# Performance work log

Measured on AMD Instinct MI355X. Metric: run time of the kernel, lower is better.

The kernel has to match this reference:

```python
import jax, jax.numpy as jnp
import numpy as np
from jax import lax
from jax.scipy.special import logsumexp

NUM_TAGS = 5
B, L = 16384, 512


def setup_inputs() -> dict:
    key = jax.random.key(0)
    k1, k2, k3, k4, k5 = jax.random.split(key, 5)
    emissions = jax.random.normal(k1, (B, L, NUM_TAGS), dtype=jnp.float32)
    tags = jax.random.randint(k2, (B, L), 0, NUM_TAGS)
    mask = jnp.ones((B, L), dtype=bool)
    # learned CRF parameters, init U(-0.1, 0.1) as in reset_parameters
    transitions = jax.random.uniform(k3, (NUM_TAGS, NUM_TAGS), minval=-0.1, maxval=0.1, dtype=jnp.float32)
    start_transitions = jax.random.uniform(k4, (NUM_TAGS,), minval=-0.1, maxval=0.1, dtype=jnp.float32)
    end_transitions = jax.random.uniform(k5, (NUM_TAGS,), minval=-0.1, maxval=0.1, dtype=jnp.float32)
    return {
        "emissions": emissions,
        "transitions": transitions,
        "start_transitions": start_transitions,
        "end_transitions": end_transitions,
        "tags": tags,
        "mask": mask,
    }


def reference(emissions, transitions, start_transitions, end_transitions, tags, mask):
    """CRF mean negative log-likelihood: log_partition - gold_score (both batch means)."""
    Bs, Ls, C = emissions.shape
    maskf = mask.astype(emissions.dtype)

    # ---- log partition (forward algorithm); note: original torch code's
    # mask application here is a no-op (where(mask, s, s)), reproduced faithfully.
    init_score = start_transitions[None, :] + emissions[:, 0]  # (B, C)

    def step(score, em_i):
        # score: (B, C) over previous tag; em_i: (B, C)
        nxt = logsumexp(score[:, :, None] + transitions[None, :, :] + em_i[:, None, :], axis=1)
        return nxt, None

    ems = jnp.swapaxes(emissions[:, 1:], 0, 1)  # (L-1, B, C)
    final_score, _ = lax.scan(step, init_score, ems)
    log_den = logsumexp(final_score + end_transitions[None, :], axis=1).mean()

    # ---- gold path score (fully vectorized over time)
    s0 = start_transitions[tags[:, 0]] + jnp.take_along_axis(emissions[:, 0], tags[:, :1], axis=1)[:, 0]
    trans_scores = transitions[tags[:, :-1], tags[:, 1:]]  # (B, L-1)
    em_at_tags = jnp.take_along_axis(emissions, tags[:, :, None], axis=2)[:, :, 0]  # (B, L)
    path_score = s0 + ((trans_scores + em_at_tags[:, 1:]) * maskf[:, 1:]).sum(axis=1)
    last_idx = mask.sum(axis=1).astype(jnp.int32) - 1  # (B,)
    last_tags = jnp.take_along_axis(tags, last_idx[:, None], axis=1)[:, 0]
    log_num = (path_score + end_transitions[last_tags]).mean()

    return log_den - log_num
```

## Files before the change

### kernel.cpp

```cpp
#include <hip/hip_runtime.h>

#define NTAGS 5
#define BATCH 16384
#define SEQL 512
#define NCHUNK 8
#define CHUNKL 64
#define TT 8
#define NTILE (CHUNKL / TT)
#define RECF 32

__device__ __forceinline__ float f4c(float4 v, int c) {
    switch (c & 3) { case 0: return v.x; case 1: return v.y; case 2: return v.z; default: return v.w; }
}
__device__ __forceinline__ int i4c(int4 v, int c) {
    switch (c & 3) { case 0: return v.x; case 1: return v.y; case 2: return v.z; default: return v.w; }
}
__device__ __forceinline__ float sel5v(float a0, float a1, float a2, float a3, float a4, int t) {
    float r = a0;
    r = (t == 1) ? a1 : r;
    r = (t == 2) ? a2 : r;
    r = (t == 3) ? a3 : r;
    r = (t == 4) ? a4 : r;
    return r;
}

struct P1State {
    float M[25];
    float logS;
    float path;
    int prev;
};

__device__ __forceinline__ void p1_tile(const float4* tb, const int4* tg, bool sk0,
                                        P1State& st, const float eT[25],
                                        const float* ldsT, const float stR[5]) {
#pragma unroll
    for (int t = 0; t < TT; ++t) {
#define EMX(j) f4c(tb[(t * 5 + (j)) >> 2], (t * 5 + (j)) & 3)
        const float e0 = EMX(0), e1 = EMX(1), e2 = EMX(2), e3 = EMX(3), e4 = EMX(4);
#undef EMX
        const int tag = i4c(tg[t >> 2], t & 3);
        if (sk0 && t == 0) {
            st.path += sel5v(stR[0], stR[1], stR[2], stR[3], stR[4], tag) +
                       sel5v(e0, e1, e2, e3, e4, tag);
            st.prev = tag;
        } else {
            const float ex0 = __expf(e0), ex1 = __expf(e1), ex2 = __expf(e2),
                        ex3 = __expf(e3), ex4 = __expf(e4);
#pragma unroll
            for (int i = 0; i < 5; ++i) {
                const float m0 = st.M[i * 5 + 0], m1 = st.M[i * 5 + 1], m2 = st.M[i * 5 + 2],
                            m3 = st.M[i * 5 + 3], m4 = st.M[i * 5 + 4];
#pragma unroll
                for (int j = 0; j < 5; ++j) {
                    float a = m0 * eT[j];
                    a = fmaf(m1, eT[5 + j], a);
                    a = fmaf(m2, eT[10 + j], a);
                    a = fmaf(m3, eT[15 + j], a);
                    a = fmaf(m4, eT[20 + j], a);
                    const float exj = (j == 0) ? ex0 : (j == 1) ? ex1 : (j == 2) ? ex2
                                     : (j == 3) ? ex3 : ex4;
                    st.M[i * 5 + j] = a * exj;
                }
            }
            st.path += ldsT[st.prev * 5 + tag] + sel5v(e0, e1, e2, e3, e4, tag);
            st.prev = tag;
        }
        if ((t & 3) == 3) {
            float m = st.M[0];
#pragma unroll
            for (int i = 1; i < 25; ++i) m = fmaxf(m, st.M[i]);
            st.logS += __logf(m);
            const float rc = __builtin_amdgcn_rcpf(m);
#pragma unroll
            for (int i = 0; i < 25; ++i) st.M[i] *= rc;
        }
    }
}

__global__ __launch_bounds__(256, 2) void crf_phase1(
    const float* __restrict__ emis, const float* __restrict__ trans,
    const float* __restrict__ startT, const int* __restrict__ tags,
    float* __restrict__ ws) {
    __shared__ float ldsT[25];
    const int tid = threadIdx.x;
    if (tid < 25) ldsT[tid] = trans[tid];
    __syncthreads();

    float eT[25];
#pragma unroll
    for (int i = 0; i < 25; ++i) eT[i] = __expf(trans[i]);
    float stR[5];
#pragma unroll
    for (int j = 0; j < 5; ++j) stR[j] = startT[j];

    const int gt = blockIdx.x * 256 + tid;
    const int seq = gt >> 3;
    const int chunk = gt & 7;
    const bool first = (chunk == 0);

    const float4* esrc =
        (const float4*)(emis + (size_t)seq * (SEQL * NTAGS) + chunk * (CHUNKL * NTAGS));
    const int tbase = seq * SEQL + chunk * CHUNKL;
    const int4* tsrc = (const int4*)(tags + tbase);

    P1State st;
#pragma unroll
    for (int i = 0; i < 25; ++i) st.M[i] = 0.f;
    st.M[0] = st.M[6] = st.M[12] = st.M[18] = st.M[24] = 1.f;
    st.logS = 0.f;
    st.path = 0.f;
    st.prev = 0;
    if (!first) st.prev = tags[tbase - 1];

    float4 tA[10], tB[10];
    int4 gA[2], gB[2];
#pragma unroll
    for (int k = 0; k < 10; ++k) tA[k] = esrc[k];
    gA[0] = tsrc[0];
    gA[1] = tsrc[1];

#pragma unroll 1
    for (int tp = 0; tp < NTILE; tp += 2) {
        {
            const float4* ep = esrc + (tp + 1) * 10;
#pragma unroll
            for (int k = 0; k < 10; ++k) tB[k] = ep[k];
            const int4* tq = tsrc + (tp + 1) * 2;
            gB[0] = tq[0];
            gB[1] = tq[1];
        }
        p1_tile(tA, gA, first && (tp == 0), st, eT, ldsT, stR);
        {
            const int nx = (tp + 2 < NTILE) ? tp + 2 : tp;
            const float4* ep = esrc + nx * 10;
#pragma unroll
            for (int k = 0; k < 10; ++k) tA[k] = ep[k];
            const int4* tq = tsrc + nx * 2;
            gA[0] = tq[0];
            gA[1] = tq[1];
        }
        p1_tile(tB, gB, false, st, eT, ldsT, stR);
    }

    float4* rec = (float4*)(ws + (size_t)gt * RECF);
#pragma unroll
    for (int k = 0; k < 6; ++k)
        rec[k] = make_float4(st.M[4 * k], st.M[4 * k + 1], st.M[4 * k + 2], st.M[4 * k + 3]);
    rec[6] = make_float4(st.M[24], st.logS, st.path, 0.f);
}

__device__ __forceinline__ void p2_combine(const float4 r[7], float v[5], float& logZ,
                                           float& path) {
#define MM(i, j) f4c(r[((i) * 5 + (j)) >> 2], ((i) * 5 + (j)) & 3)
    float nv[5];
#pragma unroll
    for (int j = 0; j < 5; ++j) {
        float a = v[0] * MM(0, j);
        a = fmaf(v[1], MM(1, j), a);
        a = fmaf(v[2], MM(2, j), a);
        a = fmaf(v[3], MM(3, j), a);
        a = fmaf(v[4], MM(4, j), a);
        nv[j] = a;
    }
#undef MM
    logZ += r[6].y;
    path += r[6].z;
    const float m = fmaxf(fmaxf(fmaxf(nv[0], nv[1]), fmaxf(nv[2], nv[3])), nv[4]);
    logZ += __logf(m);
    const float rc = __builtin_amdgcn_rcpf(m);
#pragma unroll
    for (int j = 0; j < 5; ++j) v[j] = nv[j] * rc;
}

__global__ __launch_bounds__(256, 1) void crf_phase2(
    const float* __restrict__ emis, const float* __restrict__ startT,
    const float* __restrict__ endT, const int* __restrict__ tags,
    const float* __restrict__ ws, float* __restrict__ out) {
    const int seq = blockIdx.x * 256 + threadIdx.x;
    const float* eb = emis + (size_t)seq * (SEQL * NTAGS);
    const float4 e03 = *(const float4*)eb;
    const float e4v = eb[4];
    const float s0 = startT[0] + e03.x, s1 = startT[1] + e03.y, s2 = startT[2] + e03.z,
                s3 = startT[3] + e03.w, s4 = startT[4] + e4v;
    const float m0 = fmaxf(fmaxf(fmaxf(s0, s1), fmaxf(s2, s3)), s4);
    float v[5] = {__expf(s0 - m0), __expf(s1 - m0), __expf(s2 - m0), __expf(s3 - m0),
                  __expf(s4 - m0)};
    float logZ = m0, path = 0.f;

    const float4* wsb = (const float4*)(ws + (size_t)seq * NCHUNK * RECF);
    float4 rA[7], rB[7];
#pragma unroll
    for (int k = 0; k < 7; ++k) rA[k] = wsb[k];

#pragma unroll 1
    for (int c = 0; c < NCHUNK; c += 2) {
#pragma unroll
        for (int k = 0; k < 7; ++k) rB[k] = wsb[(c + 1) * 8 + k];
        p2_combine(rA, v, logZ, path);
        const int nx = (c + 2 < NCHUNK) ? c + 2 : c;
#pragma unroll
        for (int k = 0; k < 7; ++k) rA[k] = wsb[nx * 8 + k];
        p2_combine(rB, v, logZ, path);
    }

    const float en0 = endT[0], en1 = endT[1], en2 = endT[2], en3 = endT[3], en4 = endT[4];
    float sden = v[0] * __expf(en0);
    sden = fmaf(v[1], __expf(en1), sden);
    sden = fmaf(v[2], __expf(en2), sden);
    sden = fmaf(v[3], __expf(en3), sden);
    sden = fmaf(v[4], __expf(en4), sden);
    const float den = logZ + __logf(sden);

    const int lastTag = tags[seq * SEQL + (SEQL - 1)];
    const float num = path + sel5v(en0, en1, en2, en3, en4, lastTag);

    float val = (den - num) * (1.0f / (float)BATCH);
#pragma unroll
    for (int off = 32; off > 0; off >>= 1) val += __shfl_xor(val, off, 64);
    if ((threadIdx.x & 63) == 0) atomicAdd(out, val);
}

extern "C" void kernel_launch(void* const* d_in, const int* in_sizes, int n_in,
                              void* d_out, int out_size, void* d_ws, size_t ws_size,
                              hipStream_t stream) {
    const float* emis = (const float*)d_in[0];
    const float* trans = (const float*)d_in[1];
    const float* startT = (const float*)d_in[2];
    const float* endT = (const float*)d_in[3];
    const int* tags = (const int*)d_in[4];
    float* out = (float*)d_out;
    float* ws = (float*)d_ws;

    hipMemsetAsync(out, 0, sizeof(float), stream);
    crf_phase1<<<dim3(BATCH * NCHUNK / 256), dim3(256), 0, stream>>>(emis, trans, startT,
                                                                     tags, ws);
    crf_phase2<<<dim3(BATCH / 256), dim3(256), 0, stream>>>(emis, startT, endT, tags, ws,
                                                            out);
}
```

Baseline: 312.1 us.

## Split sequences into 16 chunks, smaller tiles, deeper phase-2 prefetch

Phase 1 now splits each sequence into 16 chunks instead of 8 when the workspace is large enough. This doubles thread count and halves the per-thread serial chain, and the tile size drops to 4 steps with a launch bound of 4 blocks per CU. Phase 2 uses 64-thread blocks, a packed 28-float record and a 4-deep register prefetch of chunk matrices. The cost is more 5x5 matrix combines in phase 2, more workspace traffic, and a fallback path that depends on ws_size.

```diff
diff --git a/kernel.cpp b/kernel.cpp
--- a/kernel.cpp
+++ b/kernel.cpp
@@ -3,11 +3,8 @@
 #define NTAGS 5
 #define BATCH 16384
 #define SEQL 512
-#define NCHUNK 8
-#define CHUNKL 64
-#define TT 8
-#define NTILE (CHUNKL / TT)
-#define RECF 32
+#define TT 4
+#define RECF 28
 
 __device__ __forceinline__ float f4c(float4 v, int c) {
     switch (c & 3) { case 0: return v.x; case 1: return v.y; case 2: return v.z; default: return v.w; }
@@ -31,7 +28,7 @@
     int prev;
 };
 
-__device__ __forceinline__ void p1_tile(const float4* tb, const int4* tg, bool sk0,
+__device__ __forceinline__ void p1_tile(const float4* tb, const int4 tg, bool sk0,
                                         P1State& st, const float eT[25],
                                         const float* ldsT, const float stR[5]) {
 #pragma unroll
@@ -39,7 +36,7 @@
 #define EMX(j) f4c(tb[(t * 5 + (j)) >> 2], (t * 5 + (j)) & 3)
         const float e0 = EMX(0), e1 = EMX(1), e2 = EMX(2), e3 = EMX(3), e4 = EMX(4);
 #undef EMX
-        const int tag = i4c(tg[t >> 2], t & 3);
+        const int tag = i4c(tg, t);
         if (sk0 && t == 0) {
             st.path += sel5v(stR[0], stR[1], stR[2], stR[3], stR[4], tag) +
                        sel5v(e0, e1, e2, e3, e4, tag);
@@ -66,7 +63,7 @@
             st.path += ldsT[st.prev * 5 + tag] + sel5v(e0, e1, e2, e3, e4, tag);
             st.prev = tag;
         }
-        if ((t & 3) == 3) {
+        if (t == TT - 1) {
             float m = st.M[0];
 #pragma unroll
             for (int i = 1; i < 25; ++i) m = fmaxf(m, st.M[i]);
@@ -78,10 +75,13 @@
     }
 }
 
-__global__ __launch_bounds__(256, 2) void crf_phase1(
+template <int NC>
+__global__ __launch_bounds__(256, 4) void crf_phase1(
     const float* __restrict__ emis, const float* __restrict__ trans,
     const float* __restrict__ startT, const int* __restrict__ tags,
     float* __restrict__ ws) {
+    constexpr int CL = SEQL / NC;
+    constexpr int NTILE = CL / TT;
     __shared__ float ldsT[25];
     const int tid = threadIdx.x;
     if (tid < 25) ldsT[tid] = trans[tid];
@@ -95,13 +95,13 @@
     for (int j = 0; j < 5; ++j) stR[j] = startT[j];
 
     const int gt = blockIdx.x * 256 + tid;
-    const int seq = gt >> 3;
-    const int chunk = gt & 7;
+    const int seq = gt / NC;
+    const int chunk = gt % NC;
     const bool first = (chunk == 0);
 
     const float4* esrc =
-        (const float4*)(emis + (size_t)seq * (SEQL * NTAGS) + chunk * (CHUNKL * NTAGS));
-    const int tbase = seq * SEQL + chunk * CHUNKL;
+        (const float4*)(emis + (size_t)seq * (SEQL * NTAGS) + chunk * (CL * NTAGS));
+    const int tbase = seq * SEQL + chunk * CL;
     const int4* tsrc = (const int4*)(tags + tbase);
 
     P1State st;
@@ -113,32 +113,27 @@
     st.prev = 0;
     if (!first) st.prev = tags[tbase - 1];
 
-    float4 tA[10], tB[10];
-    int4 gA[2], gB[2];
-#pragma unroll
-    for (int k = 0; k < 10; ++k) tA[k] = esrc[k];
-    gA[0] = tsrc[0];
-    gA[1] = tsrc[1];
+    float4 tA[5], tB[5];
+    int4 gA, gB;
+#pragma unroll
+    for (int k = 0; k < 5; ++k) tA[k] = esrc[k];
+    gA = tsrc[0];
 
 #pragma unroll 1
     for (int tp = 0; tp < NTILE; tp += 2) {
         {
-            const float4* ep = esrc + (tp + 1) * 10;
-#pragma unroll
-            for (int k = 0; k < 10; ++k) tB[k] = ep[k];
-            const int4* tq = tsrc + (tp + 1) * 2;
-            gB[0] = tq[0];
-            gB[1] = tq[1];
+            const float4* ep = esrc + (tp + 1) * 5;
+#pragma unroll
+            for (int k = 0; k < 5; ++k) tB[k] = ep[k];
+            gB = tsrc[tp + 1];
         }
         p1_tile(tA, gA, first && (tp == 0), st, eT, ldsT, stR);
         {
             const int nx = (tp + 2 < NTILE) ? tp + 2 : tp;
-            const float4* ep = esrc + nx * 10;
-#pragma unroll
-            for (int k = 0; k < 10; ++k) tA[k] = ep[k];
-            const int4* tq = tsrc + nx * 2;
-            gA[0] = tq[0];
-            gA[1] = tq[1];
+            const float4* ep = esrc + nx * 5;
+#pragma unroll
+            for (int k = 0; k < 5; ++k) tA[k] = ep[k];
+            gA = tsrc[nx];
         }
         p1_tile(tB, gB, false, st, eT, ldsT, stR);
     }
@@ -173,12 +168,21 @@
     for (int j = 0; j < 5; ++j) v[j] = nv[j] * rc;
 }
 
-__global__ __launch_bounds__(256, 1) void crf_phase2(
+template <int NC>
+__global__ __launch_bounds__(64) void crf_phase2(
     const float* __restrict__ emis, const float* __restrict__ startT,
     const float* __restrict__ endT, const int* __restrict__ tags,
     const float* __restrict__ ws, float* __restrict__ out) {
-    const int seq = blockIdx.x * 256 + threadIdx.x;
+    const int seq = blockIdx.x * 64 + threadIdx.x;
     const float* eb = emis + (size_t)seq * (SEQL * NTAGS);
+    const float4* wsb = (const float4*)(ws + (size_t)seq * NC * RECF);
+
+    float4 r[4][7];
+#pragma unroll
+    for (int s = 0; s < 4; ++s)
+#pragma unroll
+        for (int k = 0; k < 7; ++k) r[s][k] = wsb[s * 7 + k];
+
     const float4 e03 = *(const float4*)eb;
     const float e4v = eb[4];
     const float s0 = startT[0] + e03.x, s1 = startT[1] + e03.y, s2 = startT[2] + e03.z,
@@ -188,20 +192,13 @@
                   __expf(s4 - m0)};
     float logZ = m0, path = 0.f;
 
-    const float4* wsb = (const float4*)(ws + (size_t)seq * NCHUNK * RECF);
-    float4 rA[7], rB[7];
-#pragma unroll
-    for (int k = 0; k < 7; ++k) rA[k] = wsb[k];
-
-#pragma unroll 1
-    for (int c = 0; c < NCHUNK; c += 2) {
-#pragma unroll
-        for (int k = 0; k < 7; ++k) rB[k] = wsb[(c + 1) * 8 + k];
-        p2_combine(rA, v, logZ, path);
-        const int nx = (c + 2 < NCHUNK) ? c + 2 : c;
-#pragma unroll
-        for (int k = 0; k < 7; ++k) rA[k] = wsb[nx * 8 + k];
-        p2_combine(rB, v, logZ, path);
+#pragma unroll
+    for (int c = 0; c < NC; ++c) {
+        p2_combine(r[c & 3], v, logZ, path);
+        if (c + 4 < NC) {
+#pragma unroll
+            for (int k = 0; k < 7; ++k) r[c & 3][k] = wsb[(c + 4) * 7 + k];
+        }
     }
 
     const float en0 = endT[0], en1 = endT[1], en2 = endT[2], en3 = endT[3], en4 = endT[4];
@@ -218,7 +215,7 @@
     float val = (den - num) * (1.0f / (float)BATCH);
 #pragma unroll
     for (int off = 32; off > 0; off >>= 1) val += __shfl_xor(val, off, 64);
-    if ((threadIdx.x & 63) == 0) atomicAdd(out, val);
+    if (threadIdx.x == 0) atomicAdd(out, val);
 }
 
 extern "C" void kernel_launch(void* const* d_in, const int* in_sizes, int n_in,
@@ -233,8 +230,17 @@
     float* ws = (float*)d_ws;
 
     hipMemsetAsync(out, 0, sizeof(float), stream);
-    crf_phase1<<<dim3(BATCH * NCHUNK / 256), dim3(256), 0, stream>>>(emis, trans, startT,
-                                                                     tags, ws);
-    crf_phase2<<<dim3(BATCH / 256), dim3(256), 0, stream>>>(emis, startT, endT, tags, ws,
-                                                            out);
-}
+
+    const size_t need16 = (size_t)BATCH * 16 * RECF * sizeof(float);
+    if (ws_size >= need16) {
+        crf_phase1<16><<<dim3(BATCH * 16 / 256), dim3(256), 0, stream>>>(emis, trans,
+                                                                         startT, tags, ws);
+        crf_phase2<16><<<dim3(BATCH / 64), dim3(64), 0, stream>>>(emis, startT, endT,
+                                                                  tags, ws, out);
+    } else {
+        crf_phase1<8><<<dim3(BATCH * 8 / 256), dim3(256), 0, stream>>>(emis, trans,
+                                                                       startT, tags, ws);
+        crf_phase2<8><<<dim3(BATCH / 64), dim3(64), 0, stream>>>(emis, startT, endT,
+                                                                 tags, ws, out);
+    }
+}
```

Result: slower. 516.1 us (+65.4%).

## Fuse CRF phases into one kernel with wave-level matrix-product tree reduction

Applied to the files above, without the earlier changes.

Replaces the two-kernel chunked scheme (8 chunks of 64 steps per sequence, workspace round trip) with a single kernel where each wave handles one sequence. Each lane processes 8 timesteps, and the 64 per-lane 5x5 transfer matrices are combined through a 6-level butterfly of shuffles and matrix products. Emissions and tags are staged through padded LDS to avoid bank conflicts. This removes the workspace traffic and the second launch, and gives far more parallelism per sequence. In exchange it adds redundant matrix multiplies in the butterfly and uses a large amount of LDS per block, which may limit occupancy.

```diff
diff --git a/kernel.cpp b/kernel.cpp
--- a/kernel.cpp
+++ b/kernel.cpp
@@ -3,18 +3,13 @@
 #define NTAGS 5
 #define BATCH 16384
 #define SEQL 512
-#define NCHUNK 8
-#define CHUNKL 64
-#define TT 8
-#define NTILE (CHUNKL / TT)
-#define RECF 32
-
-__device__ __forceinline__ float f4c(float4 v, int c) {
-    switch (c & 3) { case 0: return v.x; case 1: return v.y; case 2: return v.z; default: return v.w; }
-}
-__device__ __forceinline__ int i4c(int4 v, int c) {
-    switch (c & 3) { case 0: return v.x; case 1: return v.y; case 2: return v.z; default: return v.w; }
-}
+#define CL 8
+#define SEQF (SEQL * NTAGS)
+#define PADC 41
+#define SEQPF (64 * PADC)
+#define PTAG 9
+#define SEQPT (64 * PTAG)
+
 __device__ __forceinline__ float sel5v(float a0, float a1, float a2, float a3, float a4, int t) {
     float r = a0;
     r = (t == 1) ? a1 : r;
@@ -24,33 +19,78 @@
     return r;
 }
 
-struct P1State {
+__global__ __launch_bounds__(256, 2) void crf_fused(
+    const float* __restrict__ emis, const float* __restrict__ trans,
+    const float* __restrict__ startT, const float* __restrict__ endT,
+    const int* __restrict__ tags, float* __restrict__ out) {
+    __shared__ float lemis[4 * SEQPF];
+    __shared__ int ltags[4 * SEQPT];
+    __shared__ float ldsT[25];
+    __shared__ float lred[4];
+
+    const int tid = threadIdx.x;
+    const int lane = tid & 63;
+    const int wid = tid >> 6;
+
+    const float4* ge = (const float4*)(emis + (size_t)blockIdx.x * 4 * SEQF);
+#pragma unroll
+    for (int w = 0; w < 10; ++w) {
+        const int f = w * 256 + tid;
+        const float4 v = ge[f];
+        const int F = 4 * f;
+        const int s = F / SEQF;
+        const int r = F - s * SEQF;
+        const int piece = r / 40;
+        const int off = r - piece * 40;
+        float* dst = &lemis[s * SEQPF + piece * PADC + off];
+        dst[0] = v.x; dst[1] = v.y; dst[2] = v.z; dst[3] = v.w;
+    }
+    const int4* gt4 = (const int4*)(tags + (size_t)blockIdx.x * 4 * SEQL);
+#pragma unroll
+    for (int w = 0; w < 2; ++w) {
+        const int g = w * 256 + tid;
+        const int4 v = gt4[g];
+        const int T = 4 * g;
+        const int s = T >> 9;
+        const int q = T & 511;
+        const int piece = q >> 3;
+        const int j = q & 7;
+        int* dst = &ltags[s * SEQPT + piece * PTAG + j];
+        dst[0] = v.x; dst[1] = v.y; dst[2] = v.z; dst[3] = v.w;
+    }
+    if (tid < 25) ldsT[tid] = trans[tid];
+    __syncthreads();
+
+    float eT[25];
+#pragma unroll
+    for (int i = 0; i < 25; ++i) eT[i] = __expf(trans[i]);
+
+    const float* E = &lemis[wid * SEQPF + lane * PADC];
+    const int* G = &ltags[wid * SEQPT + lane * PTAG];
+
     float M[25];
-    float logS;
-    float path;
-    int prev;
-};
-
-__device__ __forceinline__ void p1_tile(const float4* tb, const int4* tg, bool sk0,
-                                        P1State& st, const float eT[25],
-                                        const float* ldsT, const float stR[5]) {
-#pragma unroll
-    for (int t = 0; t < TT; ++t) {
-#define EMX(j) f4c(tb[(t * 5 + (j)) >> 2], (t * 5 + (j)) & 3)
-        const float e0 = EMX(0), e1 = EMX(1), e2 = EMX(2), e3 = EMX(3), e4 = EMX(4);
-#undef EMX
-        const int tag = i4c(tg[t >> 2], t & 3);
-        if (sk0 && t == 0) {
-            st.path += sel5v(stR[0], stR[1], stR[2], stR[3], stR[4], tag) +
-                       sel5v(e0, e1, e2, e3, e4, tag);
-            st.prev = tag;
+#pragma unroll
+    for (int i = 0; i < 25; ++i) M[i] = 0.f;
+    M[0] = M[6] = M[12] = M[18] = M[24] = 1.f;
+    float logS = 0.f, path = 0.f;
+    int prev = (lane == 0) ? 0 : G[7 - PTAG];
+
+#pragma unroll
+    for (int t = 0; t < CL; ++t) {
+        const float e0 = E[t * 5 + 0], e1 = E[t * 5 + 1], e2 = E[t * 5 + 2],
+                    e3 = E[t * 5 + 3], e4 = E[t * 5 + 4];
+        const int tag = G[t];
+        if (lane == 0 && t == 0) {
+            path += sel5v(startT[0], startT[1], startT[2], startT[3], startT[4], tag) +
+                    sel5v(e0, e1, e2, e3, e4, tag);
+            prev = tag;
         } else {
             const float ex0 = __expf(e0), ex1 = __expf(e1), ex2 = __expf(e2),
                         ex3 = __expf(e3), ex4 = __expf(e4);
 #pragma unroll
             for (int i = 0; i < 5; ++i) {
-                const float m0 = st.M[i * 5 + 0], m1 = st.M[i * 5 + 1], m2 = st.M[i * 5 + 2],
-                            m3 = st.M[i * 5 + 3], m4 = st.M[i * 5 + 4];
+                const float m0 = M[i * 5 + 0], m1 = M[i * 5 + 1], m2 = M[i * 5 + 2],
+                            m3 = M[i * 5 + 3], m4 = M[i * 5 + 4];
 #pragma unroll
                 for (int j = 0; j < 5; ++j) {
                     float a = m0 * eT[j];
@@ -60,165 +100,93 @@
                     a = fmaf(m4, eT[20 + j], a);
                     const float exj = (j == 0) ? ex0 : (j == 1) ? ex1 : (j == 2) ? ex2
                                      : (j == 3) ? ex3 : ex4;
-                    st.M[i * 5 + j] = a * exj;
+                    M[i * 5 + j] = a * exj;
                 }
             }
-            st.path += ldsT[st.prev * 5 + tag] + sel5v(e0, e1, e2, e3, e4, tag);
-            st.prev = tag;
+            path += ldsT[prev * 5 + tag] + sel5v(e0, e1, e2, e3, e4, tag);
+            prev = tag;
         }
         if ((t & 3) == 3) {
-            float m = st.M[0];
-#pragma unroll
-            for (int i = 1; i < 25; ++i) m = fmaxf(m, st.M[i]);
-            st.logS += __logf(m);
+            float m = M[0];
+#pragma unroll
+            for (int i = 1; i < 25; ++i) m = fmaxf(m, M[i]);
+            logS += __logf(m);
             const float rc = __builtin_amdgcn_rcpf(m);
 #pragma unroll
-            for (int i = 0; i < 25; ++i) st.M[i] *= rc;
+            for (int i = 0; i < 25; ++i) M[i] *= rc;
         }
     }
-}
-
-__global__ __launch_bounds__(256, 2) void crf_phase1(
-    const float* __restrict__ emis, const float* __restrict__ trans,
-    const float* __restrict__ startT, const int* __restrict__ tags,
-    float* __restrict__ ws) {
-    __shared__ float ldsT[25];
-    const int tid = threadIdx.x;
-    if (tid < 25) ldsT[tid] = trans[tid];
+
+#pragma unroll
+    for (int lvl = 0; lvl < 6; ++lvl) {
+        const int mk = 1 << lvl;
+        float O[25];
+#pragma unroll
+        for (int i = 0; i < 25; ++i) O[i] = __shfl_xor(M[i], mk, 64);
+        const float oS = __shfl_xor(logS, mk, 64);
+        const bool hi = (lane & mk) != 0;
+        float L[25], R[25];
+#pragma unroll
+        for (int i = 0; i < 25; ++i) {
+            L[i] = hi ? O[i] : M[i];
+            R[i] = hi ? M[i] : O[i];
+        }
+        float NM[25];
+#pragma unroll
+        for (int i = 0; i < 5; ++i)
+#pragma unroll
+            for (int j = 0; j < 5; ++j) {
+                float a = L[i * 5 + 0] * R[0 * 5 + j];
+                a = fmaf(L[i * 5 + 1], R[1 * 5 + j], a);
+                a = fmaf(L[i * 5 + 2], R[2 * 5 + j], a);
+                a = fmaf(L[i * 5 + 3], R[3 * 5 + j], a);
+                a = fmaf(L[i * 5 + 4], R[4 * 5 + j], a);
+                NM[i * 5 + j] = a;
+            }
+        logS += oS;
+        float mx = NM[0];
+#pragma unroll
+        for (int i = 1; i < 25; ++i) mx = fmaxf(mx, NM[i]);
+        logS += __logf(mx);
+        const float rc = __builtin_amdgcn_rcpf(mx);
+#pragma unroll
+        for (int i = 0; i < 25; ++i) M[i] = NM[i] * rc;
+    }
+
+#pragma unroll
+    for (int o = 1; o < 64; o <<= 1) path += __shfl_xor(path, o, 64);
+
+    const float* E0 = &lemis[wid * SEQPF];
+    const float s0 = startT[0] + E0[0], s1 = startT[1] + E0[1], s2 = startT[2] + E0[2],
+                s3 = startT[3] + E0[3], s4 = startT[4] + E0[4];
+    const float m0 = fmaxf(fmaxf(fmaxf(s0, s1), fmaxf(s2, s3)), s4);
+    const float v0 = __expf(s0 - m0), v1 = __expf(s1 - m0), v2 = __expf(s2 - m0),
+                v3 = __expf(s3 - m0), v4 = __expf(s4 - m0);
+    float nv[5];
+#pragma unroll
+    for (int j = 0; j < 5; ++j) {
+        float a = v0 * M[0 * 5 + j];
+        a = fmaf(v1, M[1 * 5 + j], a);
+        a = fmaf(v2, M[2 * 5 + j], a);
+        a = fmaf(v3, M[3 * 5 + j], a);
+        a = fmaf(v4, M[4 * 5 + j], a);
+        nv[j] = a;
+    }
+    const float en0 = endT[0], en1 = endT[1], en2 = endT[2], en3 = endT[3], en4 = endT[4];
+    float sden = nv[0] * __expf(en0);
+    sden = fmaf(nv[1], __expf(en1), sden);
+    sden = fmaf(nv[2], __expf(en2), sden);
+    sden = fmaf(nv[3], __expf(en3), sden);
+    sden = fmaf(nv[4], __expf(en4), sden);
+    const float den = m0 + logS + __logf(sden);
+
+    const int lastTag = ltags[wid * SEQPT + 63 * PTAG + 7];
+    const float num = path + sel5v(en0, en1, en2, en3, en4, lastTag);
+
+    const float res = (den - num) * (1.0f / (float)BATCH);
+    if (lane == 0) lred[wid] = res;
     __syncthreads();
-
-    float eT[25];
-#pragma unroll
-    for (int i = 0; i < 25; ++i) eT[i] = __expf(trans[i]);
-    float stR[5];
-#pragma unroll
-    for (int j = 0; j < 5; ++j) stR[j] = startT[j];
-
-    const int gt = blockIdx.x * 256 + tid;
-    const int seq = gt >> 3;
-    const int chunk = gt & 7;
-    const bool first = (chunk == 0);
-
-    const float4* esrc =
-        (const float4*)(emis + (size_t)seq * (SEQL * NTAGS) + chunk * (CHUNKL * NTAGS));
-    const int tbase = seq * SEQL + chunk * CHUNKL;
-    const int4* tsrc = (const int4*)(tags + tbase);
-
-    P1State st;
-#pragma unroll
-    for (int i = 0; i < 25; ++i) st.M[i] = 0.f;
-    st.M[0] = st.M[6] = st.M[12] = st.M[18] = st.M[24] = 1.f;
-    st.logS = 0.f;
-    st.path = 0.f;
-    st.prev = 0;
-    if (!first) st.prev = tags[tbase - 1];
-
-    float4 tA[10], tB[10];
-    int4 gA[2], gB[2];
-#pragma unroll
-    for (int k = 0; k < 10; ++k) tA[k] = esrc[k];
-    gA[0] = tsrc[0];
-    gA[1] = tsrc[1];
-
-#pragma unroll 1
-    for (int tp = 0; tp < NTILE; tp += 2) {
-        {
-            const float4* ep = esrc + (tp + 1) * 10;
-#pragma unroll
-            for (int k = 0; k < 10; ++k) tB[k] = ep[k];
-            const int4* tq = tsrc + (tp + 1) * 2;
-            gB[0] = tq[0];
-            gB[1] = tq[1];
-        }
-        p1_tile(tA, gA, first && (tp == 0), st, eT, ldsT, stR);
-        {
-            const int nx = (tp + 2 < NTILE) ? tp + 2 : tp;
-            const float4* ep = esrc + nx * 10;
-#pragma unroll
-            for (int k = 0; k < 10; ++k) tA[k] = ep[k];
-            const int4* tq = tsrc + nx * 2;
-            gA[0] = tq[0];
-            gA[1] = tq[1];
-        }
-        p1_tile(tB, gB, false, st, eT, ldsT, stR);
-    }
-
-    float4* rec = (float4*)(ws + (size_t)gt * RECF);
-#pragma unroll
-    for (int k = 0; k < 6; ++k)
-        rec[k] = make_float4(st.M[4 * k], st.M[4 * k + 1], st.M[4 * k + 2], st.M[4 * k + 3]);
-    rec[6] = make_float4(st.M[24], st.logS, st.path, 0.f);
-}
-
-__device__ __forceinline__ void p2_combine(const float4 r[7], float v[5], float& logZ,
-                                           float& path) {
-#define MM(i, j) f4c(r[((i) * 5 + (j)) >> 2], ((i) * 5 + (j)) & 3)
-    float nv[5];
-#pragma unroll
-    for (int j = 0; j < 5; ++j) {
-        float a = v[0] * MM(0, j);
-        a = fmaf(v[1], MM(1, j), a);
-        a = fmaf(v[2], MM(2, j), a);
-        a = fmaf(v[3], MM(3, j), a);
-        a = fmaf(v[4], MM(4, j), a);
-        nv[j] = a;
-    }
-#undef MM
-    logZ += r[6].y;
-    path += r[6].z;
-    const float m = fmaxf(fmaxf(fmaxf(nv[0], nv[1]), fmaxf(nv[2], nv[3])), nv[4]);
-    logZ += __logf(m);
-    const float rc = __builtin_amdgcn_rcpf(m);
-#pragma unroll
-    for (int j = 0; j < 5; ++j) v[j] = nv[j] * rc;
-}
-
-__global__ __launch_bounds__(256, 1) void crf_phase2(
-    const float* __restrict__ emis, const float* __restrict__ startT,
-    const float* __restrict__ endT, const int* __restrict__ tags,
-    const float* __restrict__ ws, float* __restrict__ out) {
-    const int seq = blockIdx.x * 256 + threadIdx.x;
-    const float* eb = emis + (size_t)seq * (SEQL * NTAGS);
-    const float4 e03 = *(const float4*)eb;
-    const float e4v = eb[4];
-    const float s0 = startT[0] + e03.x, s1 = startT[1] + e03.y, s2 = startT[2] + e03.z,
-                s3 = startT[3] + e03.w, s4 = startT[4] + e4v;
-    const float m0 = fmaxf(fmaxf(fmaxf(s0, s1), fmaxf(s2, s3)), s4);
-    float v[5] = {__expf(s0 - m0), __expf(s1 - m0), __expf(s2 - m0), __expf(s3 - m0),
-                  __expf(s4 - m0)};
-    float logZ = m0, path = 0.f;
-
-    const float4* wsb = (const float4*)(ws + (size_t)seq * NCHUNK * RECF);
-    float4 rA[7], rB[7];
-#pragma unroll
-    for (int k = 0; k < 7; ++k) rA[k] = wsb[k];
-
-#pragma unroll 1
-    for (int c = 0; c < NCHUNK; c += 2) {
-#pragma unroll
-        for (int k = 0; k < 7; ++k) rB[k] = wsb[(c + 1) * 8 + k];
-        p2_combine(rA, v, logZ, path);
-        const int nx = (c + 2 < NCHUNK) ? c + 2 : c;
-#pragma unroll
-        for (int k = 0; k < 7; ++k) rA[k] = wsb[nx * 8 + k];
-        p2_combine(rB, v, logZ, path);
-    }
-
-    const float en0 = endT[0], en1 = endT[1], en2 = endT[2], en3 = endT[3], en4 = endT[4];
-    float sden = v[0] * __expf(en0);
-    sden = fmaf(v[1], __expf(en1), sden);
-    sden = fmaf(v[2], __expf(en2), sden);
-    sden = fmaf(v[3], __expf(en3), sden);
-    sden = fmaf(v[4], __expf(en4), sden);
-    const float den = logZ + __logf(sden);
-
-    const int lastTag = tags[seq * SEQL + (SEQL - 1)];
-    const float num = path + sel5v(en0, en1, en2, en3, en4, lastTag);
-
-    float val = (den - num) * (1.0f / (float)BATCH);
-#pragma unroll
-    for (int off = 32; off > 0; off >>= 1) val += __shfl_xor(val, off, 64);
-    if ((threadIdx.x & 63) == 0) atomicAdd(out, val);
+    if (tid == 0) atomicAdd(out, lred[0] + lred[1] + lred[2] + lred[3]);
 }
 
 extern "C" void kernel_launch(void* const* d_in, const int* in_sizes, int n_in,
@@ -230,11 +198,8 @@
     const float* endT = (const float*)d_in[3];
     const int* tags = (const int*)d_in[4];
     float* out = (float*)d_out;
-    float* ws = (float*)d_ws;
 
     hipMemsetAsync(out, 0, sizeof(float), stream);
-    crf_phase1<<<dim3(BATCH * NCHUNK / 256), dim3(256), 0, stream>>>(emis, trans, startT,
-                                                                     tags, ws);
-    crf_phase2<<<dim3(BATCH / 256), dim3(256), 0, stream>>>(emis, startT, endT, tags, ws,
-                                                            out);
+    crf_fused<<<dim3(BATCH / 4), dim3(256), 0, stream>>>(emis, trans, startT, endT, tags,
+                                                         out);
 }
```

Measured after the change: 307.0 us. About the same (-1.6%).
